# Kernel tuning notes

Hardware: AMD Instinct MI355X
Metric: run time of the kernel (lower is better)

Reference implementation:

```python
import jax, jax.numpy as jnp
import numpy as np

N = 50000       # nodes
E = 800000      # edges (before self-loops)
B = 1024        # graphs
D = 256         # emb = hidden = representation size
OUT = 128
NFEAT = 9       # OGB atom features
VOCAB = 100
NLAYERS = 4     # 1 + hidden_layers(2) + 1
NEG_SLOPE = 0.2


def setup_inputs() -> dict:
    key = jax.random.key(0)
    ks = jax.random.split(key, 10)
    x = jax.random.randint(ks[0], (N, NFEAT), 0, VOCAB)
    edge_index = jax.random.randint(ks[1], (2, E), 0, N)
    batch = jnp.sort(jax.random.randint(ks[2], (N,), 0, B))
    atom_emb = jax.random.normal(ks[3], (NFEAT, VOCAB, D), jnp.float32) * 0.1
    Ws = jax.random.normal(ks[4], (NLAYERS, D, D), jnp.float32) * (1.0 / np.sqrt(D))
    a_src = jax.random.normal(ks[5], (NLAYERS, D), jnp.float32) * 0.1
    a_dst = jax.random.normal(ks[6], (NLAYERS, D), jnp.float32) * 0.1
    biases = jnp.zeros((NLAYERS, D), jnp.float32)
    lin_w = jax.random.normal(ks[7], (3 * D, OUT), jnp.float32) * (1.0 / np.sqrt(3 * D))
    lin_b = jnp.zeros((OUT,), jnp.float32)
    return dict(x=x, edge_index=edge_index, batch=batch, atom_emb=atom_emb,
                Ws=Ws, a_src=a_src, a_dst=a_dst, biases=biases,
                lin_w=lin_w, lin_b=lin_b)


def _gat_layer(h, src, dst, W, asrc, adst, b):
    # PyG GATConv, heads=1: linear transform, per-edge additive attention,
    # segment softmax over incoming edges of each target, scatter-add aggregate.
    h = h @ W                                        # [N, D]
    s = jnp.einsum('nd,d->n', h, asrc)               # source-side score
    t = jnp.einsum('nd,d->n', h, adst)               # target-side score
    e = jax.nn.leaky_relu(s[src] + t[dst], NEG_SLOPE)  # [E']
    m = jax.ops.segment_max(e, dst, num_segments=N)  # segment softmax (stable)
    e = jnp.exp(e - m[dst])
    denom = jax.ops.segment_sum(e, dst, num_segments=N)
    alpha = e / denom[dst]                           # self-loops ensure denom > 0
    out = jax.ops.segment_sum(alpha[:, None] * h[src], dst, num_segments=N)
    return out + b


def reference(x, edge_index, batch, atom_emb, Ws, a_src, a_dst, biases, lin_w, lin_b):
    # AtomEncoder: sum of per-feature embedding lookups -> [N, D]
    h = atom_emb[jnp.arange(NFEAT)[:, None], x.T].sum(axis=0)
    # add self-loops once (GATConv default add_self_loops=True)
    loops = jnp.arange(N)
    src = jnp.concatenate([edge_index[0], loops])
    dst = jnp.concatenate([edge_index[1], loops])
    for l in range(NLAYERS):
        h = _gat_layer(h, src, dst, Ws[l], a_src[l], a_dst[l], biases[l])
        h = jax.nn.relu(h)
    # global mean / add / max pooling over graphs
    count = jax.ops.segment_sum(jnp.ones((N,), h.dtype), batch, num_segments=B)
    x_add = jax.ops.segment_sum(h, batch, num_segments=B)
    x_mean = x_add / jnp.maximum(count, 1.0)[:, None]
    x_max = jax.ops.segment_max(h, batch, num_segments=B)
    x_max = jnp.where(count[:, None] > 0, x_max, 0.0)
    feats = jnp.concatenate([x_mean, x_add, x_max], axis=1)  # [B, 3D]
    # dropout is identity in eval mode
    return feats @ lin_w + lin_b
```

## Files before the change

kernel.cpp:

```cpp
#include <hip/hip_runtime.h>
#include <math.h>

#define N_NODES 50000
#define N_EDGES 800000
#define NGRAPH  1024
#define D       256
#define OUTD    128
#define NFEAT   9
#define VOCABSZ 100
#define NLAYERS 4
#define NEG_SLOPE 0.2f
#define SCAN_NBLK ((N_NODES + 255) / 256)

typedef __attribute__((ext_vector_type(8))) short short8;
typedef __attribute__((ext_vector_type(4))) float f32x4;

static __device__ __forceinline__ unsigned short f2bf(float f) {
    unsigned int u = __float_as_uint(f);
    u = (u + 0x7FFFu + ((u >> 16) & 1u)) >> 16;
    return (unsigned short)u;
}
static __device__ __forceinline__ float bf2f(unsigned short u) {
    return __uint_as_float(((unsigned int)u) << 16);
}

#define GLOAD_LDS16(g, l) __builtin_amdgcn_global_load_lds( \
    (const __attribute__((address_space(1))) void*)(g), \
    (__attribute__((address_space(3))) void*)(l), 16, 0, 0)

__global__ void init_all(int* __restrict__ deg, float* __restrict__ s_all, float* __restrict__ t_all) {
    int i = blockIdx.x * blockDim.x + threadIdx.x;
    if (i < N_NODES) deg[i] = 1;
    if (i < NLAYERS * N_NODES) { s_all[i] = 0.f; t_all[i] = 0.f; }
}

__global__ void hist_dst(const int* __restrict__ dst, int* __restrict__ deg) {
    int e = blockIdx.x * blockDim.x + threadIdx.x;
    if (e < N_EDGES) atomicAdd(&deg[dst[e]], 1);
}

__global__ __launch_bounds__(256) void block_sum(const int* __restrict__ deg, int* __restrict__ bsum) {
    int i = blockIdx.x * 256 + threadIdx.x;
    int v = (i < N_NODES) ? deg[i] : 0;
    #pragma unroll
    for (int off = 32; off; off >>= 1) v += __shfl_down(v, off, 64);
    __shared__ int ws[4];
    if ((threadIdx.x & 63) == 0) ws[threadIdx.x >> 6] = v;
    __syncthreads();
    if (threadIdx.x == 0) bsum[blockIdx.x] = ws[0] + ws[1] + ws[2] + ws[3];
}

__global__ __launch_bounds__(256) void scan_bsum(int* __restrict__ bsum, int* __restrict__ rowptr) {
    __shared__ int sh[256];
    int tid = threadIdx.x;
    int v = (tid < SCAN_NBLK) ? bsum[tid] : 0;
    sh[tid] = v;
    __syncthreads();
    for (int off = 1; off < 256; off <<= 1) {
        int u = (tid >= off) ? sh[tid - off] : 0;
        __syncthreads();
        sh[tid] += u;
        __syncthreads();
    }
    if (tid < SCAN_NBLK) bsum[tid] = (tid > 0) ? sh[tid - 1] : 0;
    if (tid == SCAN_NBLK - 1) rowptr[N_NODES] = sh[tid];
}

__global__ __launch_bounds__(256) void scan_block(const int* __restrict__ deg,
                                                  const int* __restrict__ boffs,
                                                  int* __restrict__ rowptr) {
    __shared__ int sh[256];
    int tid = threadIdx.x;
    int i = blockIdx.x * 256 + tid;
    int v = (i < N_NODES) ? deg[i] : 0;
    sh[tid] = v;
    __syncthreads();
    for (int off = 1; off < 256; off <<= 1) {
        int u = (tid >= off) ? sh[tid - off] : 0;
        __syncthreads();
        sh[tid] += u;
        __syncthreads();
    }
    if (i < N_NODES) rowptr[i] = boffs[blockIdx.x] + sh[tid] - v;
}

__global__ void init_cursor(const int* __restrict__ rowptr, int* __restrict__ cursor, int* __restrict__ ssrc) {
    int v = blockIdx.x * blockDim.x + threadIdx.x;
    if (v < N_NODES) {
        int p = rowptr[v];
        cursor[v] = p + 1;
        ssrc[p] = v;
    }
}

__global__ void scatter_edges(const int* __restrict__ src, const int* __restrict__ dst,
                              int* __restrict__ cursor, int* __restrict__ ssrc) {
    int e = blockIdx.x * blockDim.x + threadIdx.x;
    if (e < N_EDGES) {
        int pos = atomicAdd(&cursor[dst[e]], 1);
        ssrc[pos] = src[e];
    }
}

__global__ __launch_bounds__(256) void wt_kernel(const float* __restrict__ W, unsigned short* __restrict__ Wt) {
    int t = blockIdx.x * 256 + threadIdx.x;
    int l = t >> 16;
    int k = (t >> 8) & 255;
    int n = t & 255;
    float v = W[t];
    Wt[(l << 16) + n * 256 + k] = f2bf(v);
}

__global__ __launch_bounds__(256) void atom_encoder(const int* __restrict__ x,
                                                    const float* __restrict__ emb,
                                                    unsigned short* __restrict__ h) {
    int node = blockIdx.x * 4 + (threadIdx.x >> 6);
    int lane = threadIdx.x & 63;
    if (node >= N_NODES) return;
    float4 acc = make_float4(0.f, 0.f, 0.f, 0.f);
    #pragma unroll
    for (int f = 0; f < NFEAT; ++f) {
        int xi = x[node * NFEAT + f];
        float4 v = *(const float4*)&emb[(size_t)(f * VOCABSZ + xi) * D + lane * 4];
        acc.x += v.x; acc.y += v.y; acc.z += v.z; acc.w += v.w;
    }
    ushort4 o;
    o.x = f2bf(acc.x); o.y = f2bf(acc.y); o.z = f2bf(acc.z); o.w = f2bf(acc.w);
    *(ushort4*)&h[node * D + lane * 4] = o;
}

#define GBM 128
#define GBN 128
#define GBK 64
__global__ __launch_bounds__(256) void gemm_bf16(const unsigned short* __restrict__ A,
                                                 const unsigned short* __restrict__ Wt,
                                                 const float* __restrict__ asrc,
                                                 const float* __restrict__ adst,
                                                 unsigned short* __restrict__ C,
                                                 float* __restrict__ s_out,
                                                 float* __restrict__ t_out) {
    __shared__ unsigned short smem[16896];
    int row0 = blockIdx.x * GBM;
    int col0 = blockIdx.y * GBN;
    int tid = threadIdx.x;
    int wid = tid >> 6;
    int lane = tid & 63;
    int wm = wid >> 1, wn = wid & 1;
    int l15 = lane & 15;
    int lhi = lane >> 4;

    int srcA[4], srcB[4];
    #pragma unroll
    for (int q = 0; q < 4; ++q) {
        int slot = (wid * 4 + q) * 64 + lane;
        int r = slot >> 3, c = slot & 7;
        int ra = row0 + r; if (ra > N_NODES - 1) ra = N_NODES - 1;
        srcA[q] = ra * D + ((c ^ (r & 7)) << 3);
        srcB[q] = (col0 + r) * D + ((c ^ (r & 7)) << 3);
    }

    f32x4 acc[4][4];
    #pragma unroll
    for (int i = 0; i < 4; ++i)
        #pragma unroll
        for (int j = 0; j < 4; ++j) acc[i][j] = (f32x4){0.f, 0.f, 0.f, 0.f};

    #pragma unroll
    for (int step = 0; step < 4; ++step) {
        int k0 = step * GBK;
        #pragma unroll
        for (int q = 0; q < 4; ++q) {
            GLOAD_LDS16(A + srcA[q] + k0, &smem[(wid * 4 + q) * 512]);
            GLOAD_LDS16(Wt + srcB[q] + k0, &smem[8192 + (wid * 4 + q) * 512]);
        }
        __syncthreads();
        const unsigned short* aS = smem;
        const unsigned short* bS = &smem[8192];
        #pragma unroll
        for (int ks = 0; ks < 2; ++ks) {
            short8 af[4], bf[4];
            #pragma unroll
            for (int m = 0; m < 4; ++m) {
                int r = wm * 64 + m * 16 + l15;
                int c = ks * 4 + lhi;
                af[m] = *(const short8*)&aS[r * GBK + ((c ^ (r & 7)) << 3)];
            }
            #pragma unroll
            for (int n = 0; n < 4; ++n) {
                int r = wn * 64 + n * 16 + l15;
                int c = ks * 4 + lhi;
                bf[n] = *(const short8*)&bS[r * GBK + ((c ^ (r & 7)) << 3)];
            }
            #pragma unroll
            for (int m = 0; m < 4; ++m)
                #pragma unroll
                for (int n = 0; n < 4; ++n)
                    acc[m][n] = __builtin_amdgcn_mfma_f32_16x16x32_bf16(af[m], bf[n], acc[m][n], 0, 0, 0);
        }
        __syncthreads();
    }

    unsigned short* c_s = smem;
    #pragma unroll
    for (int m = 0; m < 4; ++m) {
        #pragma unroll
        for (int r = 0; r < 4; ++r) {
            int lr = wm * 64 + m * 16 + lhi * 4 + r;
            #pragma unroll
            for (int n = 0; n < 4; ++n) {
                int lc = wn * 64 + n * 16 + l15;
                c_s[lr * 132 + lc] = f2bf(acc[m][n][r]);
            }
        }
    }
    __syncthreads();
    #pragma unroll
    for (int p = 0; p < 8; ++p) {
        int slot = p * 256 + tid;
        int r2 = slot >> 4;
        int c2 = slot & 15;
        int grow = row0 + r2;
        if (grow < N_NODES) {
            short8 vv = *(const short8*)&c_s[r2 * 132 + c2 * 8];
            *(short8*)&C[(size_t)grow * D + col0 + c2 * 8] = vv;
        }
    }

    float av[4], bv[4];
    #pragma unroll
    for (int n = 0; n < 4; ++n) {
        int gcol = col0 + wn * 64 + n * 16 + l15;
        av[n] = asrc[gcol];
        bv[n] = adst[gcol];
    }
    #pragma unroll
    for (int m = 0; m < 4; ++m) {
        #pragma unroll
        for (int r = 0; r < 4; ++r) {
            float ps = 0.f, pt = 0.f;
            #pragma unroll
            for (int n = 0; n < 4; ++n) {
                ps += acc[m][n][r] * av[n];
                pt += acc[m][n][r] * bv[n];
            }
            #pragma unroll
            for (int off = 1; off < 16; off <<= 1) {
                ps += __shfl_xor(ps, off, 64);
                pt += __shfl_xor(pt, off, 64);
            }
            int grow = row0 + wm * 64 + m * 16 + lhi * 4 + r;
            if (l15 == 0 && grow < N_NODES) {
                atomicAdd(&s_out[grow], ps);
                atomicAdd(&t_out[grow], pt);
            }
        }
    }
}

__global__ __launch_bounds__(256) void aggregate_kernel(const unsigned short* __restrict__ hW,
                                                        const float* __restrict__ s,
                                                        const float* __restrict__ t,
                                                        const int* __restrict__ rowptr,
                                                        const int* __restrict__ ssrc,
                                                        const float* __restrict__ bias,
                                                        unsigned short* __restrict__ hout) {
    int v = (blockIdx.x * blockDim.x + threadIdx.x) >> 6;
    int lane = threadIdx.x & 63;
    if (v >= N_NODES) return;
    int beg = rowptr[v];
    int deg = rowptr[v + 1] - beg;
    float tv = t[v];
    float m = -1e30f;
    float denom = 0.f;
    float acc[8];
    #pragma unroll
    for (int j = 0; j < 8; ++j) acc[j] = 0.f;
    int half = lane >> 5;
    int l32 = lane & 31;

    for (int base = 0; base < deg; base += 64) {
        int rem = deg - base; if (rem > 64) rem = 64;
        int u = 0; float e = -1e30f;
        if (lane < rem) {
            u = ssrc[beg + base + lane];
            float ev = s[u] + tv;
            e = (ev > 0.f) ? ev : NEG_SLOPE * ev;
        }
        float cm = e;
        #pragma unroll
        for (int off = 32; off; off >>= 1) cm = fmaxf(cm, __shfl_xor(cm, off, 64));
        float newm = fmaxf(m, cm);
        float scale = __expf(m - newm);
        float p = (lane < rem) ? __expf(e - newm) : 0.f;
        float ws = p;
        #pragma unroll
        for (int off = 32; off; off >>= 1) ws += __shfl_xor(ws, off, 64);
        denom = denom * scale + ws;
        m = newm;
        #pragma unroll
        for (int j = 0; j < 8; ++j) acc[j] *= scale;
        for (int i = 0; i < rem; i += 4) {
            int idx0 = i + half;
            int idx1 = i + 2 + half;
            float p0 = __shfl(p, idx0, 64);
            int   u0 = __shfl(u, idx0, 64);
            float p1 = __shfl(p, idx1, 64);
            int   u1 = __shfl(u, idx1, 64);
            short8 hv0 = *(const short8*)&hW[(size_t)u0 * D + l32 * 8];
            short8 hv1 = *(const short8*)&hW[(size_t)u1 * D + l32 * 8];
            #pragma unroll
            for (int j = 0; j < 8; ++j)
                acc[j] += p0 * bf2f((unsigned short)hv0[j]);
            #pragma unroll
            for (int j = 0; j < 8; ++j)
                acc[j] += p1 * bf2f((unsigned short)hv1[j]);
        }
    }
    #pragma unroll
    for (int j = 0; j < 8; ++j) acc[j] += __shfl_xor(acc[j], 32, 64);
    float inv = 1.f / denom;
    if (half == 0) {
        float4 b0 = *(const float4*)&bias[l32 * 8];
        float4 b1 = *(const float4*)&bias[l32 * 8 + 4];
        float bb[8] = {b0.x, b0.y, b0.z, b0.w, b1.x, b1.y, b1.z, b1.w};
        short8 o;
        #pragma unroll
        for (int j = 0; j < 8; ++j) {
            float val = fmaxf(acc[j] * inv + bb[j], 0.f);
            o[j] = (short)f2bf(val);
        }
        *(short8*)&hout[(size_t)v * D + l32 * 8] = o;
    }
}

__global__ void growptr_kernel(const int* __restrict__ batch, int* __restrict__ growptr) {
    int n = blockIdx.x * blockDim.x + threadIdx.x;
    if (n >= N_NODES) return;
    int b = batch[n];
    int prev = (n == 0) ? -1 : batch[n - 1];
    for (int g = prev + 1; g <= b; ++g) growptr[g] = n;
    if (n == N_NODES - 1) {
        for (int g = b + 1; g <= NGRAPH; ++g) growptr[g] = N_NODES;
    }
}

__global__ __launch_bounds__(256) void pool_kernel(const unsigned short* __restrict__ h,
                                                   const int* __restrict__ growptr,
                                                   float* __restrict__ feats) {
    int g = (blockIdx.x * blockDim.x + threadIdx.x) >> 6;
    int lane = threadIdx.x & 63;
    if (g >= NGRAPH) return;
    int beg = growptr[g], end = growptr[g + 1];
    float4 add = make_float4(0.f, 0.f, 0.f, 0.f);
    float4 mx = make_float4(-1e30f, -1e30f, -1e30f, -1e30f);
    int v = beg;
    for (; v + 4 <= end; v += 4) {
        ushort4 h0 = *(const ushort4*)&h[(size_t)(v + 0) * D + lane * 4];
        ushort4 h1 = *(const ushort4*)&h[(size_t)(v + 1) * D + lane * 4];
        ushort4 h2 = *(const ushort4*)&h[(size_t)(v + 2) * D + lane * 4];
        ushort4 h3 = *(const ushort4*)&h[(size_t)(v + 3) * D + lane * 4];
        ushort4 hs[4] = {h0, h1, h2, h3};
        #pragma unroll
        for (int q = 0; q < 4; ++q) {
            float a0 = bf2f(hs[q].x), a1 = bf2f(hs[q].y), a2 = bf2f(hs[q].z), a3 = bf2f(hs[q].w);
            add.x += a0; add.y += a1; add.z += a2; add.w += a3;
            mx.x = fmaxf(mx.x, a0); mx.y = fmaxf(mx.y, a1);
            mx.z = fmaxf(mx.z, a2); mx.w = fmaxf(mx.w, a3);
        }
    }
    for (; v < end; ++v) {
        ushort4 hv = *(const ushort4*)&h[(size_t)v * D + lane * 4];
        float a0 = bf2f(hv.x), a1 = bf2f(hv.y), a2 = bf2f(hv.z), a3 = bf2f(hv.w);
        add.x += a0; add.y += a1; add.z += a2; add.w += a3;
        mx.x = fmaxf(mx.x, a0); mx.y = fmaxf(mx.y, a1);
        mx.z = fmaxf(mx.z, a2); mx.w = fmaxf(mx.w, a3);
    }
    float cnt = (float)(end - beg);
    float invc = 1.f / fmaxf(cnt, 1.f);
    if (cnt <= 0.f) { mx = make_float4(0.f, 0.f, 0.f, 0.f); }
    float4 mean = make_float4(add.x * invc, add.y * invc, add.z * invc, add.w * invc);
    float* fr = feats + (size_t)g * 3 * D;
    *(float4*)&fr[0 * D + 4 * lane] = mean;
    *(float4*)&fr[1 * D + 4 * lane] = add;
    *(float4*)&fr[2 * D + 4 * lane] = mx;
}

#define GPB 4
__global__ __launch_bounds__(128) void final_linear(const float* __restrict__ feats,
                                                    const float* __restrict__ lw,
                                                    const float* __restrict__ lb,
                                                    float* __restrict__ out) {
    int g0 = blockIdx.x * GPB;
    int j = threadIdx.x;
    __shared__ float f[GPB][3 * D];
    #pragma unroll
    for (int q = 0; q < GPB * 3 * D / OUTD; ++q) {
        int i = q * OUTD + j;
        f[i / (3 * D)][i % (3 * D)] = feats[(size_t)g0 * 3 * D + i];
    }
    __syncthreads();
    float acc[GPB];
    float lbv = lb[j];
    #pragma unroll
    for (int g = 0; g < GPB; ++g) acc[g] = lbv;
    #pragma unroll 8
    for (int k = 0; k < 3 * D; ++k) {
        float w = lw[k * OUTD + j];
        #pragma unroll
        for (int g = 0; g < GPB; ++g)
            acc[g] += f[g][k] * w;
    }
    #pragma unroll
    for (int g = 0; g < GPB; ++g)
        out[(g0 + g) * OUTD + j] = acc[g];
}

extern "C" void kernel_launch(void* const* d_in, const int* in_sizes, int n_in,
                              void* d_out, int out_size, void* d_ws, size_t ws_size,
                              hipStream_t stream) {
    const int*   x        = (const int*)d_in[0];
    const int*   edge_idx = (const int*)d_in[1];
    const int*   batch    = (const int*)d_in[2];
    const float* atom_emb = (const float*)d_in[3];
    const float* Ws       = (const float*)d_in[4];
    const float* a_src    = (const float*)d_in[5];
    const float* a_dst    = (const float*)d_in[6];
    const float* biases   = (const float*)d_in[7];
    const float* lin_w    = (const float*)d_in[8];
    const float* lin_b    = (const float*)d_in[9];
    float* out = (float*)d_out;

    char* ws = (char*)d_ws;
    size_t off = 0;
    auto alloc = [&](size_t bytes) -> void* {
        void* p = ws + off;
        off += (bytes + 255) & ~(size_t)255;
        return p;
    };
    unsigned short* bufA  = (unsigned short*)alloc(sizeof(short) * (size_t)N_NODES * D);
    unsigned short* bufB  = (unsigned short*)alloc(sizeof(short) * (size_t)N_NODES * D);
    unsigned short* Wt    = (unsigned short*)alloc(sizeof(short) * NLAYERS * D * D);
    float* s_all  = (float*)alloc(sizeof(float) * NLAYERS * N_NODES);
    float* t_all  = (float*)alloc(sizeof(float) * NLAYERS * N_NODES);
    int*   deg    = (int*)alloc(sizeof(int) * N_NODES);
    int*   rowptr = (int*)alloc(sizeof(int) * (N_NODES + 1));
    int*   bsum   = (int*)alloc(sizeof(int) * 256);
    int*   ssrc   = (int*)alloc(sizeof(int) * (N_EDGES + N_NODES));
    int*   growp  = (int*)alloc(sizeof(int) * (NGRAPH + 1));
    float* feats  = (float*)alloc(sizeof(float) * (size_t)NGRAPH * 3 * D);

    const int* esrc = edge_idx;
    const int* edst = edge_idx + N_EDGES;

    init_all<<<(NLAYERS * N_NODES + 255) / 256, 256, 0, stream>>>(deg, s_all, t_all);
    hist_dst<<<(N_EDGES + 255) / 256, 256, 0, stream>>>(edst, deg);
    block_sum<<<SCAN_NBLK, 256, 0, stream>>>(deg, bsum);
    scan_bsum<<<1, 256, 0, stream>>>(bsum, rowptr);
    scan_block<<<SCAN_NBLK, 256, 0, stream>>>(deg, bsum, rowptr);
    init_cursor<<<(N_NODES + 255) / 256, 256, 0, stream>>>(rowptr, deg, ssrc);
    scatter_edges<<<(N_EDGES + 255) / 256, 256, 0, stream>>>(esrc, edst, deg, ssrc);

    wt_kernel<<<NLAYERS * D * D / 256, 256, 0, stream>>>(Ws, Wt);
    atom_encoder<<<(N_NODES + 3) / 4, 256, 0, stream>>>(x, atom_emb, bufA);

    for (int l = 0; l < NLAYERS; ++l) {
        dim3 ggrid((N_NODES + GBM - 1) / GBM, D / GBN);
        gemm_bf16<<<ggrid, 256, 0, stream>>>(bufA, Wt + (size_t)l * D * D,
                                             a_src + l * D, a_dst + l * D,
                                             bufB, s_all + (size_t)l * N_NODES,
                                             t_all + (size_t)l * N_NODES);
        aggregate_kernel<<<(N_NODES + 3) / 4, 256, 0, stream>>>(bufB,
                                             s_all + (size_t)l * N_NODES,
                                             t_all + (size_t)l * N_NODES,
                                             rowptr, ssrc, biases + l * D, bufA);
    }

    growptr_kernel<<<(N_NODES + 255) / 256, 256, 0, stream>>>(batch, growp);
    pool_kernel<<<(NGRAPH + 3) / 4, 256, 0, stream>>>(bufA, growp, feats);
    final_linear<<<NGRAPH / GPB, OUTD, 0, stream>>>(feats, lin_w, lin_b, out);
}
```

Measured before the change: 511.0 us.

## Compute full-width GEMM tile per block and reduce attention scores in LDS

```diff
diff --git a/kernel.cpp b/kernel.cpp
--- a/kernel.cpp
+++ b/kernel.cpp
@@ -28,10 +28,9 @@
     (const __attribute__((address_space(1))) void*)(g), \
     (__attribute__((address_space(3))) void*)(l), 16, 0, 0)
 
-__global__ void init_all(int* __restrict__ deg, float* __restrict__ s_all, float* __restrict__ t_all) {
-    int i = blockIdx.x * blockDim.x + threadIdx.x;
-    if (i < N_NODES) deg[i] = 1;
-    if (i < NLAYERS * N_NODES) { s_all[i] = 0.f; t_all[i] = 0.f; }
+__global__ void set_deg_one(int* deg) {
+    int v = blockIdx.x * blockDim.x + threadIdx.x;
+    if (v < N_NODES) deg[v] = 1;
 }
 
 __global__ void hist_dst(const int* __restrict__ dst, int* __restrict__ deg) {
@@ -68,7 +67,9 @@
 
 __global__ __launch_bounds__(256) void scan_block(const int* __restrict__ deg,
                                                   const int* __restrict__ boffs,
-                                                  int* __restrict__ rowptr) {
+                                                  int* __restrict__ rowptr,
+                                                  int* __restrict__ cursor,
+                                                  int* __restrict__ ssrc) {
     __shared__ int sh[256];
     int tid = threadIdx.x;
     int i = blockIdx.x * 256 + tid;
@@ -81,15 +82,11 @@
         sh[tid] += u;
         __syncthreads();
     }
-    if (i < N_NODES) rowptr[i] = boffs[blockIdx.x] + sh[tid] - v;
-}
-
-__global__ void init_cursor(const int* __restrict__ rowptr, int* __restrict__ cursor, int* __restrict__ ssrc) {
-    int v = blockIdx.x * blockDim.x + threadIdx.x;
-    if (v < N_NODES) {
-        int p = rowptr[v];
-        cursor[v] = p + 1;
-        ssrc[p] = v;
+    if (i < N_NODES) {
+        int p = boffs[blockIdx.x] + sh[tid] - v;
+        rowptr[i] = p;
+        cursor[i] = p + 1;
+        ssrc[p] = i;
     }
 }
 
@@ -130,33 +127,40 @@
 }
 
 #define GBM 128
-#define GBN 128
 #define GBK 64
-__global__ __launch_bounds__(256) void gemm_bf16(const unsigned short* __restrict__ A,
+__global__ __launch_bounds__(512) void gemm_bf16(const unsigned short* __restrict__ A,
                                                  const unsigned short* __restrict__ Wt,
                                                  const float* __restrict__ asrc,
                                                  const float* __restrict__ adst,
                                                  unsigned short* __restrict__ C,
                                                  float* __restrict__ s_out,
                                                  float* __restrict__ t_out) {
-    __shared__ unsigned short smem[16896];
+    __shared__ unsigned short smem[33792];
+    __shared__ float s_sh[GBM], t_sh[GBM];
     int row0 = blockIdx.x * GBM;
-    int col0 = blockIdx.y * GBN;
     int tid = threadIdx.x;
     int wid = tid >> 6;
     int lane = tid & 63;
-    int wm = wid >> 1, wn = wid & 1;
+    int wm = wid >> 2, wn = wid & 3;
     int l15 = lane & 15;
     int lhi = lane >> 4;
 
-    int srcA[4], srcB[4];
-    #pragma unroll
-    for (int q = 0; q < 4; ++q) {
-        int slot = (wid * 4 + q) * 64 + lane;
+    if (tid < GBM) s_sh[tid] = 0.f;
+    else if (tid < 2 * GBM) t_sh[tid - GBM] = 0.f;
+
+    int srcA[2], srcB[4];
+    #pragma unroll
+    for (int q = 0; q < 2; ++q) {
+        int slot = q * 512 + tid;
         int r = slot >> 3, c = slot & 7;
         int ra = row0 + r; if (ra > N_NODES - 1) ra = N_NODES - 1;
         srcA[q] = ra * D + ((c ^ (r & 7)) << 3);
-        srcB[q] = (col0 + r) * D + ((c ^ (r & 7)) << 3);
+    }
+    #pragma unroll
+    for (int q = 0; q < 4; ++q) {
+        int slot = q * 512 + tid;
+        int r = slot >> 3, c = slot & 7;
+        srcB[q] = r * D + ((c ^ (r & 7)) << 3);
     }
 
     f32x4 acc[4][4];
@@ -169,13 +173,12 @@
     for (int step = 0; step < 4; ++step) {
         int k0 = step * GBK;
         #pragma unroll
-        for (int q = 0; q < 4; ++q) {
-            GLOAD_LDS16(A + srcA[q] + k0, &smem[(wid * 4 + q) * 512]);
-            GLOAD_LDS16(Wt + srcB[q] + k0, &smem[8192 + (wid * 4 + q) * 512]);
-        }
-        __syncthreads();
-        const unsigned short* aS = smem;
-        const unsigned short* bS = &smem[8192];
+        for (int q = 0; q < 2; ++q)
+            GLOAD_LDS16(A + srcA[q] + k0, &smem[(q * 512 + wid * 64) * 8]);
+        #pragma unroll
+        for (int q = 0; q < 4; ++q)
+            GLOAD_LDS16(Wt + srcB[q] + k0, &smem[8192 + (q * 512 + wid * 64) * 8]);
+        __syncthreads();
         #pragma unroll
         for (int ks = 0; ks < 2; ++ks) {
             short8 af[4], bf[4];
@@ -183,13 +186,13 @@
             for (int m = 0; m < 4; ++m) {
                 int r = wm * 64 + m * 16 + l15;
                 int c = ks * 4 + lhi;
-                af[m] = *(const short8*)&aS[r * GBK + ((c ^ (r & 7)) << 3)];
+                af[m] = *(const short8*)&smem[r * GBK + ((c ^ (r & 7)) << 3)];
             }
             #pragma unroll
             for (int n = 0; n < 4; ++n) {
                 int r = wn * 64 + n * 16 + l15;
                 int c = ks * 4 + lhi;
-                bf[n] = *(const short8*)&bS[r * GBK + ((c ^ (r & 7)) << 3)];
+                bf[n] = *(const short8*)&smem[8192 + r * GBK + ((c ^ (r & 7)) << 3)];
             }
             #pragma unroll
             for (int m = 0; m < 4; ++m)
@@ -209,27 +212,27 @@
             #pragma unroll
             for (int n = 0; n < 4; ++n) {
                 int lc = wn * 64 + n * 16 + l15;
-                c_s[lr * 132 + lc] = f2bf(acc[m][n][r]);
+                c_s[lr * 264 + lc] = f2bf(acc[m][n][r]);
             }
         }
     }
     __syncthreads();
     #pragma unroll
     for (int p = 0; p < 8; ++p) {
-        int slot = p * 256 + tid;
-        int r2 = slot >> 4;
-        int c2 = slot & 15;
+        int slot = p * 512 + tid;
+        int r2 = slot >> 5;
+        int c2 = slot & 31;
         int grow = row0 + r2;
         if (grow < N_NODES) {
-            short8 vv = *(const short8*)&c_s[r2 * 132 + c2 * 8];
-            *(short8*)&C[(size_t)grow * D + col0 + c2 * 8] = vv;
+            short8 vv = *(const short8*)&c_s[r2 * 264 + c2 * 8];
+            *(short8*)&C[(size_t)grow * D + c2 * 8] = vv;
         }
     }
 
     float av[4], bv[4];
     #pragma unroll
     for (int n = 0; n < 4; ++n) {
-        int gcol = col0 + wn * 64 + n * 16 + l15;
+        int gcol = wn * 64 + n * 16 + l15;
         av[n] = asrc[gcol];
         bv[n] = adst[gcol];
     }
@@ -248,12 +251,20 @@
                 ps += __shfl_xor(ps, off, 64);
                 pt += __shfl_xor(pt, off, 64);
             }
-            int grow = row0 + wm * 64 + m * 16 + lhi * 4 + r;
-            if (l15 == 0 && grow < N_NODES) {
-                atomicAdd(&s_out[grow], ps);
-                atomicAdd(&t_out[grow], pt);
-            }
-        }
+            if (l15 == 0) {
+                int lr = wm * 64 + m * 16 + lhi * 4 + r;
+                atomicAdd(&s_sh[lr], ps);
+                atomicAdd(&t_sh[lr], pt);
+            }
+        }
+    }
+    __syncthreads();
+    if (tid < GBM) {
+        int gr = row0 + tid;
+        if (gr < N_NODES) s_out[gr] = s_sh[tid];
+    } else if (tid < 2 * GBM) {
+        int gr = row0 + tid - GBM;
+        if (gr < N_NODES) t_out[gr] = t_sh[tid - GBM];
     }
 }
 
@@ -440,8 +451,8 @@
     unsigned short* bufA  = (unsigned short*)alloc(sizeof(short) * (size_t)N_NODES * D);
     unsigned short* bufB  = (unsigned short*)alloc(sizeof(short) * (size_t)N_NODES * D);
     unsigned short* Wt    = (unsigned short*)alloc(sizeof(short) * NLAYERS * D * D);
-    float* s_all  = (float*)alloc(sizeof(float) * NLAYERS * N_NODES);
-    float* t_all  = (float*)alloc(sizeof(float) * NLAYERS * N_NODES);
+    float* s      = (float*)alloc(sizeof(float) * N_NODES);
+    float* t      = (float*)alloc(sizeof(float) * N_NODES);
     int*   deg    = (int*)alloc(sizeof(int) * N_NODES);
     int*   rowptr = (int*)alloc(sizeof(int) * (N_NODES + 1));
     int*   bsum   = (int*)alloc(sizeof(int) * 256);
@@ -452,26 +463,22 @@
     const int* esrc = edge_idx;
     const int* edst = edge_idx + N_EDGES;
 
-    init_all<<<(NLAYERS * N_NODES + 255) / 256, 256, 0, stream>>>(deg, s_all, t_all);
+    set_deg_one<<<(N_NODES + 255) / 256, 256, 0, stream>>>(deg);
     hist_dst<<<(N_EDGES + 255) / 256, 256, 0, stream>>>(edst, deg);
     block_sum<<<SCAN_NBLK, 256, 0, stream>>>(deg, bsum);
     scan_bsum<<<1, 256, 0, stream>>>(bsum, rowptr);
-    scan_block<<<SCAN_NBLK, 256, 0, stream>>>(deg, bsum, rowptr);
-    init_cursor<<<(N_NODES + 255) / 256, 256, 0, stream>>>(rowptr, deg, ssrc);
+    scan_block<<<SCAN_NBLK, 256, 0, stream>>>(deg, bsum, rowptr, deg, ssrc);
     scatter_edges<<<(N_EDGES + 255) / 256, 256, 0, stream>>>(esrc, edst, deg, ssrc);
 
     wt_kernel<<<NLAYERS * D * D / 256, 256, 0, stream>>>(Ws, Wt);
     atom_encoder<<<(N_NODES + 3) / 4, 256, 0, stream>>>(x, atom_emb, bufA);
 
     for (int l = 0; l < NLAYERS; ++l) {
-        dim3 ggrid((N_NODES + GBM - 1) / GBM, D / GBN);
-        gemm_bf16<<<ggrid, 256, 0, stream>>>(bufA, Wt + (size_t)l * D * D,
+        gemm_bf16<<<(N_NODES + GBM - 1) / GBM, 512, 0, stream>>>(
+                                             bufA, Wt + (size_t)l * D * D,
                                              a_src + l * D, a_dst + l * D,
-                                             bufB, s_all + (size_t)l * N_NODES,
-                                             t_all + (size_t)l * N_NODES);
-        aggregate_kernel<<<(N_NODES + 3) / 4, 256, 0, stream>>>(bufB,
-                                             s_all + (size_t)l * N_NODES,
-                                             t_all + (size_t)l * N_NODES,
+                                             bufB, s, t);
+        aggregate_kernel<<<(N_NODES + 3) / 4, 256, 0, stream>>>(bufB, s, t,
                                              rowptr, ssrc, biases + l * D, bufA);
     }
 
```

After: 519.2 us. No clear change (+1.6%).
